# Kernel optimization log

Measured on AMD Instinct MI355X. Metric: run time of the kernel, lower is better.

Reference implementation:

```python
import jax, jax.numpy as jnp
import numpy as np

B, L, H = 16, 4096, 1024  # batch, encoder length, hidden_size


def setup_inputs() -> dict:
    key = jax.random.key(0)
    k1, k2, k3, k4, k5 = jax.random.split(key, 5)
    s = 1.0 / np.sqrt(H)
    return {
        "hidden": jax.random.normal(k1, (B, H // 2), dtype=jnp.float32),
        "encoder_outputs": jax.random.normal(k2, (B, L, H), dtype=jnp.float32),
        "attn_w": jax.random.normal(k3, (2 * H, H), dtype=jnp.float32) * s,
        "attn_b": jax.random.normal(k4, (H,), dtype=jnp.float32) * s,
        "v_w": jax.random.normal(k5, (H,), dtype=jnp.float32) * s,
    }


def reference(hidden, encoder_outputs, attn_w, attn_b, v_w):
    Hd = encoder_outputs.shape[-1]
    # torch: repeated_hidden = hidden.unsqueeze(1).repeat(1, L, 2) -> tile hidden twice on feature dim
    rep_h = jnp.concatenate([hidden, hidden], axis=-1)  # (B, H)
    # Decompose attn Linear over the concat [rep_h, enc] to avoid materializing (B, L, 2H):
    w_h, w_e = attn_w[:Hd], attn_w[Hd:]  # (H, H) each
    proj_h = rep_h @ w_h + attn_b                       # (B, H), broadcast over L
    proj_e = jnp.einsum("blh,hk->blk", encoder_outputs, w_e)  # (B, L, H)
    energy = jnp.tanh(proj_h[:, None, :] + proj_e)      # (B, L, H)
    scores = jnp.einsum("blh,h->bl", energy, v_w)       # (B, L)
    weights = jax.nn.softmax(scores, axis=1)            # (B, L)
    context = jnp.einsum("blh,bl->bh", encoder_outputs, weights)  # (B, H)
    return context
```

## Files before the change

kernel.cpp:

```cpp
#include <hip/hip_runtime.h>
#include <hip/hip_bf16.h>
#include <math.h>

#define BB 16
#define LL 4096
#define HH 1024

#define OFF_PH   (2u << 20)
#define OFF_SC   (OFF_PH + 65536u)
#define OFF_WT   (OFF_SC + 262144u)

typedef short s16x8 __attribute__((ext_vector_type(8)));
typedef float f32x4 __attribute__((ext_vector_type(4)));

__device__ __forceinline__ unsigned short f2bf(float f) {
  unsigned int x = __float_as_uint(f);
  unsigned int r = (x + 0x7FFFu + ((x >> 16) & 1u)) >> 16;
  return (unsigned short)r;
}
__device__ __forceinline__ unsigned int pack2(float a, float b) {
  return (unsigned int)f2bf(a) | ((unsigned int)f2bf(b) << 16);
}
__device__ __forceinline__ void glds16(const void* g, void* l) {
  __builtin_amdgcn_global_load_lds((const unsigned int*)g, (unsigned int*)l, 16, 0, 0);
}

__global__ void zerok(float* out) {
  out[blockIdx.x * 1024 + threadIdx.x] = 0.0f;
}

__global__ void projhk(const float* __restrict__ hidden, const float* __restrict__ attn_w,
                       const float* __restrict__ attn_b, float* __restrict__ ph) {
  const int b = blockIdx.x >> 2;
  const int h = (blockIdx.x & 3) * 256 + threadIdx.x;
  const float* hid = hidden + b * 512;
  float acc = attn_b[h];
#pragma unroll 8
  for (int k = 0; k < 1024; ++k)
    acc += hid[k & 511] * attn_w[k * HH + h];
  ph[b * HH + h] = acc;
}

__global__ void wimgk(const float* __restrict__ attn_w, unsigned char* __restrict__ img) {
  const int step = blockIdx.x >> 4;
  const int nt   = blockIdx.x & 15;
  const int t    = threadIdx.x;
  const int nl = t & 63, kg = t >> 6;
  const int n = nt * 64 + nl;
  unsigned short u[8];
#pragma unroll
  for (int j = 0; j < 8; ++j) {
    float f = attn_w[(size_t)(1024 + step * 32 + kg * 8 + j) * HH + n];
    u[j] = f2bf(f);
  }
  uint4 p;
  p.x = (unsigned int)u[0] | ((unsigned int)u[1] << 16);
  p.y = (unsigned int)u[2] | ((unsigned int)u[3] << 16);
  p.z = (unsigned int)u[4] | ((unsigned int)u[5] << 16);
  p.w = (unsigned int)u[6] | ((unsigned int)u[7] << 16);
  unsigned int off = ((unsigned int)(n * 64 + kg * 16)) ^ ((unsigned int)(n & 7) << 4);
  *(uint4*)(img + (size_t)step * 65536 + off) = p;
}

__global__ __launch_bounds__(512, 2) void scorek(
    const float* __restrict__ enc, const unsigned char* __restrict__ wimg,
    const float* __restrict__ ph, const float* __restrict__ vw,
    float* __restrict__ scores) {
  __shared__ __align__(16) unsigned char wlds[2][65536];
  __shared__ __align__(16) unsigned char elds[2][8192];
  __shared__ float red[64];

  const int t = threadIdx.x;
  const int lane = t & 63;
  const int wave = t >> 6;
  const int kg = lane >> 4;
  const int lr = lane & 15;
  const int g0 = blockIdx.x << 6;
  const int bidx = g0 >> 12;

  if (t < 64) red[t] = 0.0f;

  const int em = t >> 3;
  const int ek = t & 7;
  const float* encbase = enc + (size_t)(g0 + em) * HH + ek * 8;
  const int ewoff = ((em * 128 + ek * 16) ^ ((em & 7) << 4));

  const int exr = (lr & 7) << 4;
  int aoff[4];
#pragma unroll
  for (int mf = 0; mf < 4; ++mf)
    aoff[mf] = (((mf * 16 + lr) * 128 + kg * 16) ^ exr);
  int boff[8];
#pragma unroll
  for (int nf = 0; nf < 8; ++nf)
    boff[nf] = (((wave * 128 + nf * 16 + lr) * 64 + kg * 16) ^ exr);

  f32x4 acc[4][8];
#pragma unroll
  for (int mf = 0; mf < 4; ++mf)
#pragma unroll
    for (int nf = 0; nf < 8; ++nf)
      acc[mf][nf] = (f32x4){0.f, 0.f, 0.f, 0.f};

  float4 er0, er1;

  {
#pragma unroll
    for (int i = 0; i < 8; ++i)
      glds16(wimg + t * 16 + i * 8192, &wlds[0][t * 16 + i * 8192]);
    er0 = *(const float4*)(encbase);
    er1 = *(const float4*)(encbase + 4);
    uint4 p;
    p.x = pack2(er0.x, er0.y); p.y = pack2(er0.z, er0.w);
    p.z = pack2(er1.x, er1.y); p.w = pack2(er1.z, er1.w);
    *(uint4*)(&elds[0][ewoff]) = p;
    __syncthreads();
  }

#pragma unroll 1
  for (int s2 = 0; s2 < 16; ++s2) {
    {
      const unsigned char* src = wimg + (size_t)(2 * s2 + 1) * 65536;
#pragma unroll
      for (int i = 0; i < 8; ++i)
        glds16(src + t * 16 + i * 8192, &wlds[1][t * 16 + i * 8192]);
      if (s2 < 15) {
        er0 = *(const float4*)(encbase + (s2 + 1) * 64);
        er1 = *(const float4*)(encbase + (s2 + 1) * 64 + 4);
      }
      const unsigned char* wb = wlds[0];
      const unsigned char* eb = elds[s2 & 1];
      s16x8 a[4];
#pragma unroll
      for (int mf = 0; mf < 4; ++mf)
        a[mf] = *(const s16x8*)(eb + aoff[mf]);
#pragma unroll
      for (int nf = 0; nf < 8; ++nf) {
        s16x8 b = *(const s16x8*)(wb + boff[nf]);
#pragma unroll
        for (int mf = 0; mf < 4; ++mf)
          acc[mf][nf] = __builtin_amdgcn_mfma_f32_16x16x32_bf16(a[mf], b, acc[mf][nf], 0, 0, 0);
      }
      __syncthreads();
    }
    {
      if (s2 < 15) {
        uint4 p;
        p.x = pack2(er0.x, er0.y); p.y = pack2(er0.z, er0.w);
        p.z = pack2(er1.x, er1.y); p.w = pack2(er1.z, er1.w);
        *(uint4*)(&elds[(s2 + 1) & 1][ewoff]) = p;
        const unsigned char* src = wimg + (size_t)(2 * s2 + 2) * 65536;
#pragma unroll
        for (int i = 0; i < 8; ++i)
          glds16(src + t * 16 + i * 8192, &wlds[0][t * 16 + i * 8192]);
      }
      const unsigned char* wb = wlds[1];
      const unsigned char* eb = elds[s2 & 1];
      s16x8 a[4];
#pragma unroll
      for (int mf = 0; mf < 4; ++mf)
        a[mf] = *(const s16x8*)(eb + (aoff[mf] ^ 64));
#pragma unroll
      for (int nf = 0; nf < 8; ++nf) {
        s16x8 b = *(const s16x8*)(wb + boff[nf]);
#pragma unroll
        for (int mf = 0; mf < 4; ++mf)
          acc[mf][nf] = __builtin_amdgcn_mfma_f32_16x16x32_bf16(a[mf], b, acc[mf][nf], 0, 0, 0);
      }
      __syncthreads();
    }
  }

  float phv[8], vwv[8];
#pragma unroll
  for (int nf = 0; nf < 8; ++nf) {
    int col = wave * 128 + nf * 16 + lr;
    phv[nf] = ph[bidx * HH + col];
    vwv[nf] = vw[col];
  }
  float part[4][4];
#pragma unroll
  for (int mf = 0; mf < 4; ++mf) {
#pragma unroll
    for (int i = 0; i < 4; ++i) {
      float s = 0.f;
#pragma unroll
      for (int nf = 0; nf < 8; ++nf)
        s += vwv[nf] * tanhf(acc[mf][nf][i] + phv[nf]);
      part[mf][i] = s;
    }
  }
#pragma unroll
  for (int mask = 1; mask < 16; mask <<= 1) {
#pragma unroll
    for (int mf = 0; mf < 4; ++mf)
#pragma unroll
      for (int i = 0; i < 4; ++i)
        part[mf][i] += __shfl_xor(part[mf][i], mask, 64);
  }
  if (lr == 0) {
#pragma unroll
    for (int mf = 0; mf < 4; ++mf)
#pragma unroll
      for (int i = 0; i < 4; ++i)
        atomicAdd(&red[mf * 16 + kg * 4 + i], part[mf][i]);
  }
  __syncthreads();
  if (t < 64) scores[g0 + t] = red[t];
}

__global__ void smaxk(const float* __restrict__ sc, float* __restrict__ wt) {
  const int b = blockIdx.x, t = threadIdx.x;
  const float* s = sc + b * LL;
  float v[16];
#pragma unroll
  for (int i = 0; i < 4; ++i) {
    float4 f = *(const float4*)(s + t * 16 + i * 4);
    v[i * 4 + 0] = f.x; v[i * 4 + 1] = f.y; v[i * 4 + 2] = f.z; v[i * 4 + 3] = f.w;
  }
  float m = -1e30f;
#pragma unroll
  for (int i = 0; i < 16; ++i) m = fmaxf(m, v[i]);
#pragma unroll
  for (int off = 1; off < 64; off <<= 1) m = fmaxf(m, __shfl_xor(m, off, 64));
  __shared__ float wm[4], wsm[4];
  const int wv = t >> 6, ln = t & 63;
  if (ln == 0) wm[wv] = m;
  __syncthreads();
  m = fmaxf(fmaxf(wm[0], wm[1]), fmaxf(wm[2], wm[3]));
  float sum = 0.f;
#pragma unroll
  for (int i = 0; i < 16; ++i) { v[i] = expf(v[i] - m); sum += v[i]; }
#pragma unroll
  for (int off = 1; off < 64; off <<= 1) sum += __shfl_xor(sum, off, 64);
  if (ln == 0) wsm[wv] = sum;
  __syncthreads();
  sum = wsm[0] + wsm[1] + wsm[2] + wsm[3];
  const float inv = 1.0f / sum;
#pragma unroll
  for (int i = 0; i < 4; ++i) {
    float4 f;
    f.x = v[i * 4 + 0] * inv; f.y = v[i * 4 + 1] * inv;
    f.z = v[i * 4 + 2] * inv; f.w = v[i * 4 + 3] * inv;
    *(float4*)(wt + b * LL + t * 16 + i * 4) = f;
  }
}

__global__ void ctxk(const float* __restrict__ enc, const float* __restrict__ wt,
                     float* __restrict__ out) {
  const int bid = blockIdx.x;
  const int b = bid >> 6;
  const int l0 = (bid & 63) * 64;
  const int t = threadIdx.x;
  __shared__ float wl[64];
  if (t < 64) wl[t] = wt[b * LL + l0 + t];
  __syncthreads();
  const float* base = enc + (size_t)(b * LL + l0) * HH + t * 4;
  float ax = 0.f, ay = 0.f, az = 0.f, aw = 0.f;
#pragma unroll 4
  for (int l = 0; l < 64; ++l) {
    float4 e = *(const float4*)(base + (size_t)l * HH);
    float w = wl[l];
    ax += w * e.x; ay += w * e.y; az += w * e.z; aw += w * e.w;
  }
  float* o = out + b * HH + t * 4;
  atomicAdd(o + 0, ax); atomicAdd(o + 1, ay);
  atomicAdd(o + 2, az); atomicAdd(o + 3, aw);
}

extern "C" void kernel_launch(void* const* d_in, const int* in_sizes, int n_in,
                              void* d_out, int out_size, void* d_ws, size_t ws_size,
                              hipStream_t stream) {
  (void)in_sizes; (void)n_in; (void)out_size; (void)ws_size;
  const float* hidden = (const float*)d_in[0];
  const float* enc    = (const float*)d_in[1];
  const float* attn_w = (const float*)d_in[2];
  const float* attn_b = (const float*)d_in[3];
  const float* v_w    = (const float*)d_in[4];
  float* out = (float*)d_out;
  unsigned char* ws = (unsigned char*)d_ws;

  unsigned char* wimg = ws;
  float* ph     = (float*)(ws + OFF_PH);
  float* scores = (float*)(ws + OFF_SC);
  float* wts    = (float*)(ws + OFF_WT);

  zerok<<<dim3(16), dim3(1024), 0, stream>>>(out);
  projhk<<<dim3(64), dim3(256), 0, stream>>>(hidden, attn_w, attn_b, ph);
  wimgk<<<dim3(512), dim3(256), 0, stream>>>(attn_w, wimg);
  scorek<<<dim3(1024), dim3(512), 0, stream>>>(enc, wimg, ph, v_w, scores);
  smaxk<<<dim3(16), dim3(256), 0, stream>>>(scores, wts);
  ctxk<<<dim3(1024), dim3(256), 0, stream>>>(enc, wts, out);
}
```

Measured before the change: 687.0 us.

## Deepen score GEMM pipeline, use fast tanh, replace atomic context reduction

The score kernel's main loop is reworked so encoder chunks are prefetched two steps ahead into registers. It uses explicit waitcnt and s_barrier instead of __syncthreads, and raises wave priority around the MFMA block. tanhf is replaced by an exp/rcp approximation, and bf16 packing uses native conversions. The context kernel drops atomics and the zeroing kernel in favour of a two-pass partial-sum reduction. This reuses the weight-image workspace region, which is safe only because the score kernel has already finished with it.

```diff
diff --git a/kernel.cpp b/kernel.cpp
--- a/kernel.cpp
+++ b/kernel.cpp
@@ -18,15 +18,18 @@
   unsigned int r = (x + 0x7FFFu + ((x >> 16) & 1u)) >> 16;
   return (unsigned short)r;
 }
-__device__ __forceinline__ unsigned int pack2(float a, float b) {
-  return (unsigned int)f2bf(a) | ((unsigned int)f2bf(b) << 16);
-}
 __device__ __forceinline__ void glds16(const void* g, void* l) {
   __builtin_amdgcn_global_load_lds((const unsigned int*)g, (unsigned int*)l, 16, 0, 0);
 }
-
-__global__ void zerok(float* out) {
-  out[blockIdx.x * 1024 + threadIdx.x] = 0.0f;
+__device__ __forceinline__ uint4 pack8(float4 u, float4 v) {
+  union { uint4 q; __bf16 h[8]; } r;
+  r.h[0] = (__bf16)u.x; r.h[1] = (__bf16)u.y; r.h[2] = (__bf16)u.z; r.h[3] = (__bf16)u.w;
+  r.h[4] = (__bf16)v.x; r.h[5] = (__bf16)v.y; r.h[6] = (__bf16)v.z; r.h[7] = (__bf16)v.w;
+  return r.q;
+}
+__device__ __forceinline__ float fast_tanh(float x) {
+  float e = __expf(2.0f * x);
+  return 1.0f - 2.0f * __builtin_amdgcn_rcpf(e + 1.0f);
 }
 
 __global__ void projhk(const float* __restrict__ hidden, const float* __restrict__ attn_w,
@@ -102,74 +105,73 @@
     for (int nf = 0; nf < 8; ++nf)
       acc[mf][nf] = (f32x4){0.f, 0.f, 0.f, 0.f};
 
-  float4 er0, er1;
+  float4 ea0, ea1, eb0, eb1;
 
   {
 #pragma unroll
     for (int i = 0; i < 8; ++i)
       glds16(wimg + t * 16 + i * 8192, &wlds[0][t * 16 + i * 8192]);
-    er0 = *(const float4*)(encbase);
-    er1 = *(const float4*)(encbase + 4);
-    uint4 p;
-    p.x = pack2(er0.x, er0.y); p.y = pack2(er0.z, er0.w);
-    p.z = pack2(er1.x, er1.y); p.w = pack2(er1.z, er1.w);
-    *(uint4*)(&elds[0][ewoff]) = p;
-    __syncthreads();
-  }
+    ea0 = *(const float4*)(encbase);
+    ea1 = *(const float4*)(encbase + 4);
+    eb0 = *(const float4*)(encbase + 64);
+    eb1 = *(const float4*)(encbase + 64 + 4);
+    asm volatile("s_waitcnt vmcnt(2)" ::: "memory");
+    __builtin_amdgcn_sched_barrier(0);
+    *(uint4*)(&elds[0][ewoff]) = pack8(ea0, ea1);
+    asm volatile("s_waitcnt lgkmcnt(0)" ::: "memory");
+    __builtin_amdgcn_s_barrier();
+  }
+
+#define ISSUE_W(dstbuf) do { \
+    const unsigned char* wsrc_ = wimg + ((size_t)((s + 1) & 31) << 16); \
+    _Pragma("unroll") \
+    for (int i = 0; i < 8; ++i) \
+      glds16(wsrc_ + t * 16 + i * 8192, &wlds[dstbuf][t * 16 + i * 8192]); \
+  } while (0)
+
+#define LOAD_ENC(r0, r1) do { \
+    int ck_ = ((s >> 1) + 2) & 15; \
+    r0 = *(const float4*)(encbase + ck_ * 64); \
+    r1 = *(const float4*)(encbase + ck_ * 64 + 4); \
+  } while (0)
+
+#define WRITE_ENC(dstbuf, r0, r1) do { \
+    *(uint4*)(&elds[dstbuf][ewoff]) = pack8(r0, r1); \
+  } while (0)
+
+#define COMPUTE(wbuf, ebuf, kh) do { \
+    asm volatile("s_waitcnt vmcnt(10)" ::: "memory"); \
+    __builtin_amdgcn_sched_barrier(0); \
+    const unsigned char* wb_ = wlds[wbuf]; \
+    const unsigned char* eb_ = elds[ebuf]; \
+    s16x8 a_[4]; \
+    _Pragma("unroll") \
+    for (int mf = 0; mf < 4; ++mf) a_[mf] = *(const s16x8*)(eb_ + (aoff[mf] ^ (kh))); \
+    __builtin_amdgcn_s_setprio(1); \
+    _Pragma("unroll") \
+    for (int nf = 0; nf < 8; ++nf) { \
+      s16x8 b_ = *(const s16x8*)(wb_ + boff[nf]); \
+      _Pragma("unroll") \
+      for (int mf = 0; mf < 4; ++mf) \
+        acc[mf][nf] = __builtin_amdgcn_mfma_f32_16x16x32_bf16(a_[mf], b_, acc[mf][nf], 0, 0, 0); \
+    } \
+    __builtin_amdgcn_s_setprio(0); \
+    asm volatile("s_waitcnt lgkmcnt(0)" ::: "memory"); \
+    __builtin_amdgcn_s_barrier(); \
+  } while (0)
 
 #pragma unroll 1
-  for (int s2 = 0; s2 < 16; ++s2) {
-    {
-      const unsigned char* src = wimg + (size_t)(2 * s2 + 1) * 65536;
-#pragma unroll
-      for (int i = 0; i < 8; ++i)
-        glds16(src + t * 16 + i * 8192, &wlds[1][t * 16 + i * 8192]);
-      if (s2 < 15) {
-        er0 = *(const float4*)(encbase + (s2 + 1) * 64);
-        er1 = *(const float4*)(encbase + (s2 + 1) * 64 + 4);
-      }
-      const unsigned char* wb = wlds[0];
-      const unsigned char* eb = elds[s2 & 1];
-      s16x8 a[4];
-#pragma unroll
-      for (int mf = 0; mf < 4; ++mf)
-        a[mf] = *(const s16x8*)(eb + aoff[mf]);
-#pragma unroll
-      for (int nf = 0; nf < 8; ++nf) {
-        s16x8 b = *(const s16x8*)(wb + boff[nf]);
-#pragma unroll
-        for (int mf = 0; mf < 4; ++mf)
-          acc[mf][nf] = __builtin_amdgcn_mfma_f32_16x16x32_bf16(a[mf], b, acc[mf][nf], 0, 0, 0);
-      }
-      __syncthreads();
-    }
-    {
-      if (s2 < 15) {
-        uint4 p;
-        p.x = pack2(er0.x, er0.y); p.y = pack2(er0.z, er0.w);
-        p.z = pack2(er1.x, er1.y); p.w = pack2(er1.z, er1.w);
-        *(uint4*)(&elds[(s2 + 1) & 1][ewoff]) = p;
-        const unsigned char* src = wimg + (size_t)(2 * s2 + 2) * 65536;
-#pragma unroll
-        for (int i = 0; i < 8; ++i)
-          glds16(src + t * 16 + i * 8192, &wlds[0][t * 16 + i * 8192]);
-      }
-      const unsigned char* wb = wlds[1];
-      const unsigned char* eb = elds[s2 & 1];
-      s16x8 a[4];
-#pragma unroll
-      for (int mf = 0; mf < 4; ++mf)
-        a[mf] = *(const s16x8*)(eb + (aoff[mf] ^ 64));
-#pragma unroll
-      for (int nf = 0; nf < 8; ++nf) {
-        s16x8 b = *(const s16x8*)(wb + boff[nf]);
-#pragma unroll
-        for (int mf = 0; mf < 4; ++mf)
-          acc[mf][nf] = __builtin_amdgcn_mfma_f32_16x16x32_bf16(a[mf], b, acc[mf][nf], 0, 0, 0);
-      }
-      __syncthreads();
-    }
-  }
+  for (int s4 = 0; s4 < 8; ++s4) {
+    int s;
+    s = s4 * 4 + 0; ISSUE_W(1); LOAD_ENC(ea0, ea1);  COMPUTE(0, 0, 0);
+    s = s4 * 4 + 1; ISSUE_W(0); WRITE_ENC(1, eb0, eb1); COMPUTE(1, 0, 64);
+    s = s4 * 4 + 2; ISSUE_W(1); LOAD_ENC(eb0, eb1);  COMPUTE(0, 1, 0);
+    s = s4 * 4 + 3; ISSUE_W(0); WRITE_ENC(0, ea0, ea1); COMPUTE(1, 1, 64);
+  }
+#undef ISSUE_W
+#undef LOAD_ENC
+#undef WRITE_ENC
+#undef COMPUTE
 
   float phv[8], vwv[8];
 #pragma unroll
@@ -186,7 +188,7 @@
       float s = 0.f;
 #pragma unroll
       for (int nf = 0; nf < 8; ++nf)
-        s += vwv[nf] * tanhf(acc[mf][nf][i] + phv[nf]);
+        s += vwv[nf] * fast_tanh(acc[mf][nf][i] + phv[nf]);
       part[mf][i] = s;
     }
   }
@@ -246,26 +248,36 @@
   }
 }
 
-__global__ void ctxk(const float* __restrict__ enc, const float* __restrict__ wt,
-                     float* __restrict__ out) {
-  const int bid = blockIdx.x;
-  const int b = bid >> 6;
-  const int l0 = (bid & 63) * 64;
+__global__ void ctxk1(const float* __restrict__ enc, const float* __restrict__ wt,
+                      float* __restrict__ part) {
+  const int b = blockIdx.x >> 5;
+  const int lc = blockIdx.x & 31;
   const int t = threadIdx.x;
-  __shared__ float wl[64];
-  if (t < 64) wl[t] = wt[b * LL + l0 + t];
+  __shared__ float wl[128];
+  if (t < 128) wl[t] = wt[b * LL + lc * 128 + t];
   __syncthreads();
-  const float* base = enc + (size_t)(b * LL + l0) * HH + t * 4;
+  const float* base = enc + ((size_t)(b * LL + lc * 128)) * HH + t * 4;
   float ax = 0.f, ay = 0.f, az = 0.f, aw = 0.f;
-#pragma unroll 4
-  for (int l = 0; l < 64; ++l) {
+#pragma unroll 8
+  for (int l = 0; l < 128; ++l) {
     float4 e = *(const float4*)(base + (size_t)l * HH);
     float w = wl[l];
     ax += w * e.x; ay += w * e.y; az += w * e.z; aw += w * e.w;
   }
-  float* o = out + b * HH + t * 4;
-  atomicAdd(o + 0, ax); atomicAdd(o + 1, ay);
-  atomicAdd(o + 2, az); atomicAdd(o + 3, aw);
+  float4 r; r.x = ax; r.y = ay; r.z = az; r.w = aw;
+  *(float4*)(part + (size_t)blockIdx.x * HH + t * 4) = r;
+}
+
+__global__ void ctxk2(const float* __restrict__ part, float* __restrict__ out) {
+  const int b = blockIdx.x, t = threadIdx.x;
+  float ax = 0.f, ay = 0.f, az = 0.f, aw = 0.f;
+#pragma unroll
+  for (int j = 0; j < 32; ++j) {
+    float4 p = *(const float4*)(part + (size_t)(b * 32 + j) * HH + t * 4);
+    ax += p.x; ay += p.y; az += p.z; aw += p.w;
+  }
+  float4 r; r.x = ax; r.y = ay; r.z = az; r.w = aw;
+  *(float4*)(out + b * HH + t * 4) = r;
 }
 
 extern "C" void kernel_launch(void* const* d_in, const int* in_sizes, int n_in,
@@ -281,14 +293,15 @@
   unsigned char* ws = (unsigned char*)d_ws;
 
   unsigned char* wimg = ws;
+  float* cpart  = (float*)ws;
   float* ph     = (float*)(ws + OFF_PH);
   float* scores = (float*)(ws + OFF_SC);
   float* wts    = (float*)(ws + OFF_WT);
 
-  zerok<<<dim3(16), dim3(1024), 0, stream>>>(out);
   projhk<<<dim3(64), dim3(256), 0, stream>>>(hidden, attn_w, attn_b, ph);
   wimgk<<<dim3(512), dim3(256), 0, stream>>>(attn_w, wimg);
   scorek<<<dim3(1024), dim3(512), 0, stream>>>(enc, wimg, ph, v_w, scores);
   smaxk<<<dim3(16), dim3(256), 0, stream>>>(scores, wts);
-  ctxk<<<dim3(1024), dim3(256), 0, stream>>>(enc, wts, out);
-}
+  ctxk1<<<dim3(512), dim3(256), 0, stream>>>(enc, wts, cpart);
+  ctxk2<<<dim3(16), dim3(256), 0, stream>>>(cpart, out);
+}
```

After: 623.6 us. 1.1x faster.
